# Kernel optimization log

Hardware: AMD Instinct MI355X
Metric: run time of the kernel (lower is better)

Reference implementation:

```python
import jax, jax.numpy as jnp
import numpy as np
from jax import lax

L, H, DH, D, FF = 8, 16, 64, 1024, 4096  # layers, heads, head dim, model dim, mlp hidden
B, S = 4, 512
EPS = 1e-5


def setup_inputs() -> dict:
    key = jax.random.key(0)
    ks = jax.random.split(key, 8)
    std = 0.02
    return {
        "x": jax.random.normal(ks[0], (B, S, D), jnp.float32),
        "ln1_w": jnp.ones((L, D), jnp.float32),
        "ln1_b": jnp.zeros((L, D), jnp.float32),
        "qw": jax.random.normal(ks[1], (L, H, DH, DH), jnp.float32) * std,
        "qb": jnp.zeros((L, H, DH), jnp.float32),
        "kw": jax.random.normal(ks[2], (L, H, DH, DH), jnp.float32) * std,
        "kb": jnp.zeros((L, H, DH), jnp.float32),
        "vw": jax.random.normal(ks[3], (L, H, DH, DH), jnp.float32) * std,
        "vb": jnp.zeros((L, H, DH), jnp.float32),
        "ln2_w": jnp.ones((L, D), jnp.float32),
        "ln2_b": jnp.zeros((L, D), jnp.float32),
        "w1": jax.random.normal(ks[4], (L, D, FF), jnp.float32) * std,
        "b1": jnp.zeros((L, FF), jnp.float32),
        "w2": jax.random.normal(ks[5], (L, FF, D), jnp.float32) * std,
        "b2": jnp.zeros((L, D), jnp.float32),
    }


def _layernorm(x, w, b):
    m = jnp.mean(x, axis=-1, keepdims=True)
    v = jnp.mean(jnp.square(x - m), axis=-1, keepdims=True)
    return (x - m) * lax.rsqrt(v + EPS) * w + b


def reference(x, ln1_w, ln1_b, qw, qb, kw, kb, vw, vb, ln2_w, ln2_b, w1, b1, w2, b2):
    b, s, d = x.shape
    scale = 1.0 / jnp.sqrt(jnp.asarray(DH, x.dtype))

    def layer(h, p):
        (l1w, l1b, Qw, Qb, Kw, Kb, Vw, Vb, l2w, l2b, W1, B1, W2, B2) = p
        y = _layernorm(h, l1w, l1b)
        yh = y.reshape(b, s, H, DH)
        # nn.Linear per head: y @ W.T + b, W is [out=e, in=d]
        q = jnp.einsum('bshd,hed->bshe', yh, Qw) + Qb
        k = jnp.einsum('bshd,hed->bshe', yh, Kw) + Kb
        v = jnp.einsum('bshd,hed->bshe', yh, Vw) + Vb
        attn = jax.nn.softmax(jnp.einsum('bshe,bthe->bhst', q, k) * scale, axis=-1)
        o = jnp.einsum('bhst,bthe->bshe', attn, v).reshape(b, s, d)
        h = h + o
        z = _layernorm(h, l2w, l2b)
        z = jax.nn.gelu(z @ W1 + B1, approximate=False) @ W2 + B2
        return h + z, None

    params = (ln1_w, ln1_b, qw, qb, kw, kb, vw, vb, ln2_w, ln2_b, w1, b1, w2, b2)
    out, _ = lax.scan(layer, x, params)
    return out
```

## Files before the change

kernel.cpp:

```cpp
#include <hip/hip_runtime.h>
#include <hip/hip_bf16.h>

typedef __hip_bfloat16 bf16;
typedef __bf16 bf16x8 __attribute__((ext_vector_type(8)));
typedef float f32x4 __attribute__((ext_vector_type(4)));
typedef unsigned short u16;
typedef unsigned int u32;

#define SEQ 512
#define DMODEL 1024
#define FFDIM 4096
#define NHEAD 16
#define HDIM 64
#define NB 4
#define NLAYER 8

#define SBAR() asm volatile("s_barrier" ::: "memory")

__device__ __forceinline__ u16 f2bu(float f) {
    union { bf16 h; u16 u; } c; c.h = __float2bfloat16(f); return c.u;
}

__device__ __forceinline__ void gload16(const bf16* g, bf16* l) {
    __builtin_amdgcn_global_load_lds(
        (const __attribute__((address_space(1))) unsigned int*)g,
        (__attribute__((address_space(3))) unsigned int*)l,
        16, 0, 0);
}

__device__ __forceinline__ void gemm_pipe(
    const bf16* __restrict__ A, int lda,
    const bf16* __restrict__ B, int ldb,
    int nkt,
    f32x4 (&acc)[8][2],
    char* lA, char* lB)
{
    const int tid = threadIdx.x;
    const int lane = tid & 63;
    const int wave = tid >> 6;
    const int wr = wave >> 2, wc = wave & 3;
    const int l15 = lane & 15, l4 = lane >> 4;

    auto stage = [&](int c, int t) {
        const bf16* Ak = A + t * 64;
        const bf16* Bk = B + t * 64;
        bf16* dA = (bf16*)(lA + c * 32768);
        bf16* dB = (bf16*)(lB + c * 16384);
#pragma unroll
        for (int it = 0; it < 4; ++it) {
            const int e = (it * 512 + tid) * 8;
            const int r = e >> 6;
            const int cb = (e & 63) * 2;
            const int sc = (cb ^ (((r >> 2) & 1) << 5)) >> 1;
            gload16(Ak + (long)r * lda + sc, dA + e);
        }
#pragma unroll
        for (int it = 0; it < 2; ++it) {
            const int e = (it * 512 + tid) * 8;
            const int r = e >> 6;
            const int cb = (e & 63) * 2;
            const int sc = (cb ^ (((r >> 2) & 1) << 5)) >> 1;
            gload16(Bk + (long)r * ldb + sc, dB + e);
        }
    };

    stage(0, 0);
    stage(1, 1);
    asm volatile("s_waitcnt vmcnt(6)" ::: "memory");
    SBAR();

    for (int t = 0; t < nkt; ++t) {
        const int cur = t & 1;
        const char* bA = lA + cur * 32768;
        const char* bB = lB + cur * 16384;

        bf16x8 bf_[2][2];
#pragma unroll
        for (int fn = 0; fn < 2; ++fn)
#pragma unroll
            for (int ks = 0; ks < 2; ++ks) {
                const int row = wc * 32 + fn * 16 + l15;
                int byte = row * 128 + (ks * 32 + l4 * 8) * 2;
                byte ^= ((row >> 2) & 1) << 5;
                bf_[fn][ks] = *(const bf16x8*)(bB + byte);
            }
#pragma unroll
        for (int q = 0; q < 4; ++q) {
            bf16x8 af[2][2];
#pragma unroll
            for (int i = 0; i < 2; ++i)
#pragma unroll
                for (int ks = 0; ks < 2; ++ks) {
                    const int row = wr * 128 + (q * 2 + i) * 16 + l15;
                    int byte = row * 128 + (ks * 32 + l4 * 8) * 2;
                    byte ^= ((row >> 2) & 1) << 5;
                    af[i][ks] = *(const bf16x8*)(bA + byte);
                }
            __builtin_amdgcn_s_setprio(1);
#pragma unroll
            for (int i = 0; i < 2; ++i)
#pragma unroll
                for (int fn = 0; fn < 2; ++fn)
#pragma unroll
                    for (int ks = 0; ks < 2; ++ks)
                        acc[q * 2 + i][fn] = __builtin_amdgcn_mfma_f32_16x16x32_bf16(
                            af[i][ks], bf_[fn][ks], acc[q * 2 + i][fn], 0, 0, 0);
            __builtin_amdgcn_s_setprio(0);
        }
        SBAR();
        if (t + 2 < nkt) {
            stage(cur, t + 2);
            asm volatile("s_waitcnt vmcnt(6)" ::: "memory");
        } else {
            asm volatile("s_waitcnt vmcnt(0)" ::: "memory");
        }
        SBAR();
    }
}

__global__ __launch_bounds__(256) void k_ln(const float* __restrict__ h,
                                            const float* __restrict__ w,
                                            const float* __restrict__ bp,
                                            bf16* __restrict__ out)
{
    const int row = blockIdx.x;
    const int tid = threadIdx.x;
    const float4 x = ((const float4*)(h + (long)row * DMODEL))[tid];
    float s  = x.x + x.y + x.z + x.w;
    float s2 = x.x * x.x + x.y * x.y + x.z * x.z + x.w * x.w;
#pragma unroll
    for (int off = 32; off; off >>= 1) { s += __shfl_xor(s, off); s2 += __shfl_xor(s2, off); }
    __shared__ float rs[4], rs2[4];
    const int wave = tid >> 6;
    if ((tid & 63) == 0) { rs[wave] = s; rs2[wave] = s2; }
    __syncthreads();
    const float S1 = rs[0] + rs[1] + rs[2] + rs[3];
    const float S2 = rs2[0] + rs2[1] + rs2[2] + rs2[3];
    const float mean = S1 * (1.0f / DMODEL);
    const float var  = S2 * (1.0f / DMODEL) - mean * mean;
    const float rstd = rsqrtf(var + 1e-5f);
    const float4 wv = ((const float4*)w)[tid];
    const float4 bv = ((const float4*)bp)[tid];
    uint2 o;
    o.x = (u32)f2bu((x.x - mean) * rstd * wv.x + bv.x) |
          ((u32)f2bu((x.y - mean) * rstd * wv.y + bv.y) << 16);
    o.y = (u32)f2bu((x.z - mean) * rstd * wv.z + bv.z) |
          ((u32)f2bu((x.w - mean) * rstd * wv.w + bv.w) << 16);
    ((uint2*)(out + (long)row * DMODEL))[tid] = o;
}

__global__ __launch_bounds__(256) void k_transw_all(const float* __restrict__ w1,
                                                    const float* __restrict__ w2,
                                                    bf16* __restrict__ w1t,
                                                    bf16* __restrict__ w2t)
{
    int bid = blockIdx.x;
    const int l = bid >> 11;
    bid &= 2047;
    const long lofs = (long)l * DMODEL * FFDIM;
    const float* src; bf16* dst; int R, C, rb, cb;
    if (bid < 1024) {
        src = w1 + lofs; dst = w1t + lofs; R = DMODEL; C = FFDIM;
        rb = (bid >> 6) << 6; cb = (bid & 63) << 6;
    } else {
        bid -= 1024;
        src = w2 + lofs; dst = w2t + lofs; R = FFDIM; C = DMODEL;
        rb = (bid >> 4) << 6; cb = (bid & 15) << 6;
    }
    const int tid = threadIdx.x;
    const int lane = tid & 63, wave = tid >> 6;
    const int r0 = ((wave & 1) << 5) + ((lane >> 3) << 2);
    const int c0 = ((wave >> 1) << 5) + ((lane & 7) << 2);

    float4 v[4];
#pragma unroll
    for (int i = 0; i < 4; ++i)
        v[i] = *(const float4*)(src + (long)(rb + r0 + i) * C + cb + c0);
#pragma unroll
    for (int j = 0; j < 4; ++j) {
        const float a0 = (&v[0].x)[j], a1 = (&v[1].x)[j];
        const float a2 = (&v[2].x)[j], a3 = (&v[3].x)[j];
        uint2 o;
        o.x = (u32)f2bu(a0) | ((u32)f2bu(a1) << 16);
        o.y = (u32)f2bu(a2) | ((u32)f2bu(a3) << 16);
        *(uint2*)(dst + (long)(cb + c0 + j) * R + rb + r0) = o;
    }
}

__global__ __launch_bounds__(256) void k_qkv2(const bf16* __restrict__ y,
                                              const float* __restrict__ qwl,
                                              const float* __restrict__ kwl,
                                              const float* __restrict__ vwl,
                                              const float* __restrict__ qb,
                                              const float* __restrict__ kb,
                                              const float* __restrict__ vb,
                                              bf16* __restrict__ qh,
                                              bf16* __restrict__ kh,
                                              bf16* __restrict__ vt)
{
    __shared__ __align__(16) char lmem[128 * 64 * 2 + 64 * 64 * 2];
    bf16* lA = (bf16*)lmem;
    char* lBb = lmem + 128 * 64 * 2;

    const int tid = threadIdx.x;
    const int lane = tid & 63, wave = tid >> 6;
    const int l15 = lane & 15, l4 = lane >> 4;
    const int z = blockIdx.y;
    const int b = z >> 4, hd = z & 15;
    const bf16* A = y + (long)b * SEQ * DMODEL + hd * HDIM + (long)blockIdx.x * 128 * DMODEL;

#pragma unroll
    for (int it = 0; it < 4; ++it) {
        const int f = (it * 256 + tid) * 8;
        const int r = f >> 6, c = f & 63;
        gload16(A + (long)r * DMODEL + c, lA + f);
    }
    __syncthreads();

    bf16x8 qa[2][2];
#pragma unroll
    for (int fm = 0; fm < 2; ++fm)
#pragma unroll
        for (int ks = 0; ks < 2; ++ks)
            qa[fm][ks] = *(const bf16x8*)(lA + (wave * 32 + fm * 16 + l15) * 64 + ks * 32 + l4 * 8);

    for (int t = 0; t < 3; ++t) {
        __syncthreads();
        const float* Bsrc = ((t == 0) ? qwl : (t == 1) ? kwl : vwl) + (long)hd * HDIM * HDIM;
#pragma unroll
        for (int it = 0; it < 4; ++it) {
            const int f = (it * 256 + tid) * 4;
            const float4 v = *(const float4*)(Bsrc + f);
            uint2 o;
            o.x = (u32)f2bu(v.x) | ((u32)f2bu(v.y) << 16);
            o.y = (u32)f2bu(v.z) | ((u32)f2bu(v.w) << 16);
            const int row = f >> 6;
            const int byte = (f << 1) ^ ((row & 7) << 4);
            *(uint2*)(lBb + byte) = o;
        }
        __syncthreads();

        bf16x8 bfr[4][2];
#pragma unroll
        for (int fn = 0; fn < 4; ++fn)
#pragma unroll
            for (int ks = 0; ks < 2; ++ks) {
                const int row = fn * 16 + l15;
                int byte = (row << 7) + ((ks * 32 + l4 * 8) << 1);
                byte ^= (row & 7) << 4;
                bfr[fn][ks] = *(const bf16x8*)(lBb + byte);
            }
        f32x4 acc[2][4] = {};
#pragma unroll
        for (int ks = 0; ks < 2; ++ks)
#pragma unroll
            for (int fm = 0; fm < 2; ++fm)
#pragma unroll
                for (int fn = 0; fn < 4; ++fn)
                    acc[fm][fn] = __builtin_amdgcn_mfma_f32_16x16x32_bf16(
                        qa[fm][ks], bfr[fn][ks], acc[fm][fn], 0, 0, 0);

        const float* bias = (t == 0) ? qb : (t == 1) ? kb : vb;
#pragma unroll
        for (int fm = 0; fm < 2; ++fm)
#pragma unroll
            for (int fn = 0; fn < 4; ++fn)
#pragma unroll
                for (int r = 0; r < 4; ++r) {
                    const int srow = blockIdx.x * 128 + wave * 32 + fm * 16 + l4 * 4 + r;
                    const int e = fn * 16 + l15;
                    float v = acc[fm][fn][r] + bias[hd * HDIM + e];
                    if (t == 0) {
                        qh[((long)z * SEQ + srow) * HDIM + e] = __float2bfloat16(v * 0.125f);
                    } else if (t == 1) {
                        kh[((long)z * SEQ + srow) * HDIM + e] = __float2bfloat16(v);
                    } else {
                        vt[((long)z * HDIM + e) * SEQ + srow] = __float2bfloat16(v);
                    }
                }
    }
}

__global__ __launch_bounds__(256) void k_flash(const bf16* __restrict__ qh,
                                               const bf16* __restrict__ kh,
                                               const bf16* __restrict__ vt,
                                               float* __restrict__ h)
{
    __shared__ __align__(16) char lmem[24576];
    bf16* lQ = (bf16*)lmem;
    char* lKb = lmem + 8192;
    char* lVb = lmem + 16384;

    const int tid = threadIdx.x;
    const int lane = tid & 63, wave = tid >> 6;
    const int l15 = lane & 15, l4 = lane >> 4;
    const int z = blockIdx.y;
    const int b = z >> 4, hd = z & 15;
    const int q0 = blockIdx.x * 64;

    const bf16* Qsrc = qh + ((long)z * SEQ + q0) * HDIM;
#pragma unroll
    for (int it = 0; it < 2; ++it) {
        const int f = (it * 256 + tid) * 8;
        gload16(Qsrc + f, lQ + f);
    }
    __syncthreads();

    bf16x8 qa[2];
#pragma unroll
    for (int ks = 0; ks < 2; ++ks)
        qa[ks] = *(const bf16x8*)(lQ + (wave * 16 + l15) * 64 + ks * 32 + l4 * 8);

    char* lPb = lmem + wave * 2048;

    f32x4 O[4] = {};
    float mrun[4], lrun[4];
#pragma unroll
    for (int r = 0; r < 4; ++r) { mrun[r] = -1e30f; lrun[r] = 0.0f; }

    for (int kv = 0; kv < SEQ / 64; ++kv) {
        __syncthreads();
        const bf16* Ksrc = kh + ((long)z * SEQ + kv * 64) * HDIM;
#pragma unroll
        for (int it = 0; it < 2; ++it) {
            const int f = (it * 256 + tid) * 8;
            const int r = f >> 6;
            const uint4 v = *(const uint4*)(Ksrc + f);
            *(uint4*)(lKb + ((f << 1) ^ ((r & 7) << 4))) = v;
        }
        const bf16* Vsrc = vt + (long)z * HDIM * SEQ + kv * 64;
#pragma unroll
        for (int it = 0; it < 2; ++it) {
            const int f = (it * 256 + tid) * 8;
            const int r = f >> 6, c = f & 63;
            const uint4 v = *(const uint4*)(Vsrc + (long)r * SEQ + c);
            *(uint4*)(lVb + ((f << 1) ^ ((r & 7) << 4))) = v;
        }
        __syncthreads();

        f32x4 sa[4];
#pragma unroll
        for (int fn = 0; fn < 4; ++fn) sa[fn] = (f32x4){0.f, 0.f, 0.f, 0.f};
#pragma unroll
        for (int ks = 0; ks < 2; ++ks)
#pragma unroll
            for (int fn = 0; fn < 4; ++fn) {
                const int row = fn * 16 + l15;
                int byte = (row << 7) + ((ks * 32 + l4 * 8) << 1);
                byte ^= (row & 7) << 4;
                const bf16x8 kb_ = *(const bf16x8*)(lKb + byte);
                sa[fn] = __builtin_amdgcn_mfma_f32_16x16x32_bf16(qa[ks], kb_, sa[fn], 0, 0, 0);
            }

#pragma unroll
        for (int r = 0; r < 4; ++r) {
            float mx = fmaxf(fmaxf(sa[0][r], sa[1][r]), fmaxf(sa[2][r], sa[3][r]));
#pragma unroll
            for (int m_ = 1; m_ < 16; m_ <<= 1) mx = fmaxf(mx, __shfl_xor(mx, m_));
            const float nm = fmaxf(mrun[r], mx);
            const float al = __expf(mrun[r] - nm);
            mrun[r] = nm;
            float p0 = __expf(sa[0][r] - nm), p1 = __expf(sa[1][r] - nm);
            float p2 = __expf(sa[2][r] - nm), p3 = __expf(sa[3][r] - nm);
            float ps = p0 + p1 + p2 + p3;
#pragma unroll
            for (int m_ = 1; m_ < 16; m_ <<= 1) ps += __shfl_xor(ps, m_);
            lrun[r] = lrun[r] * al + ps;
#pragma unroll
            for (int fn = 0; fn < 4; ++fn) O[fn][r] *= al;
            const int row = l4 * 4 + r;
            const int rsw = (row & 7) << 4;
            const int rb = row << 7;
            *(u16*)(lPb + ((rb + ((0 * 16 + l15) << 1)) ^ rsw)) = f2bu(p0);
            *(u16*)(lPb + ((rb + ((1 * 16 + l15) << 1)) ^ rsw)) = f2bu(p1);
            *(u16*)(lPb + ((rb + ((2 * 16 + l15) << 1)) ^ rsw)) = f2bu(p2);
            *(u16*)(lPb + ((rb + ((3 * 16 + l15) << 1)) ^ rsw)) = f2bu(p3);
        }

#pragma unroll
        for (int ks = 0; ks < 2; ++ks) {
            const int rowp = l15;
            int pbyte = (rowp << 7) + ((ks * 32 + l4 * 8) << 1);
            pbyte ^= (rowp & 7) << 4;
            const bf16x8 pa = *(const bf16x8*)(lPb + pbyte);
#pragma unroll
            for (int fn = 0; fn < 4; ++fn) {
                const int row = fn * 16 + l15;
                int byte = (row << 7) + ((ks * 32 + l4 * 8) << 1);
                byte ^= (row & 7) << 4;
                const bf16x8 vb_ = *(const bf16x8*)(lVb + byte);
                O[fn] = __builtin_amdgcn_mfma_f32_16x16x32_bf16(pa, vb_, O[fn], 0, 0, 0);
            }
        }
    }

    float rinv[4];
#pragma unroll
    for (int r = 0; r < 4; ++r) rinv[r] = 1.0f / lrun[r];
#pragma unroll
    for (int fn = 0; fn < 4; ++fn)
#pragma unroll
        for (int r = 0; r < 4; ++r) {
            const int srow = q0 + wave * 16 + l4 * 4 + r;
            const int e = fn * 16 + l15;
            h[((long)b * SEQ + srow) * DMODEL + hd * HDIM + e] += O[fn][r] * rinv[r];
        }
}

__global__ __launch_bounds__(512, 2) void k_gemm1(const bf16* __restrict__ zb,
                                                  const bf16* __restrict__ w1t,
                                                  const float* __restrict__ b1,
                                                  bf16* __restrict__ ff1)
{
    __shared__ __align__(16) char lmem[98304];
    const bf16* A = zb + (long)blockIdx.x * 256 * DMODEL;
    const bf16* B = w1t + (long)blockIdx.y * 128 * DMODEL;
    f32x4 acc[8][2] = {};
    gemm_pipe(A, DMODEL, B, DMODEL, DMODEL / 64, acc, lmem, lmem + 65536);

    const int lane = threadIdx.x & 63, wave = threadIdx.x >> 6;
    const int wr = wave >> 2, wc = wave & 3;
    const int l15 = lane & 15, l4 = lane >> 4;
#pragma unroll
    for (int fm = 0; fm < 8; ++fm)
#pragma unroll
        for (int fn = 0; fn < 2; ++fn)
#pragma unroll
            for (int r = 0; r < 4; ++r) {
                const int row = blockIdx.x * 256 + wr * 128 + fm * 16 + l4 * 4 + r;
                const int col = blockIdx.y * 128 + wc * 32 + fn * 16 + l15;
                const float x = acc[fm][fn][r] + b1[col];
                const float g = 0.5f * x * (1.0f + erff(x * 0.70710678118f));
                ff1[(long)row * FFDIM + col] = __float2bfloat16(g);
            }
}

__global__ __launch_bounds__(512, 2) void k_gemm2(const bf16* __restrict__ ff1,
                                                  const bf16* __restrict__ w2t,
                                                  float* __restrict__ part)
{
    __shared__ __align__(16) char lmem[98304];
    const int sk = blockIdx.z;
    const bf16* A = ff1 + (long)blockIdx.x * 256 * FFDIM + (long)sk * 1024;
    const bf16* B = w2t + (long)blockIdx.y * 128 * FFDIM + (long)sk * 1024;
    f32x4 acc[8][2] = {};
    gemm_pipe(A, FFDIM, B, FFDIM, 1024 / 64, acc, lmem, lmem + 65536);

    float* out = part + (long)sk * (NB * SEQ) * DMODEL;
    const int lane = threadIdx.x & 63, wave = threadIdx.x >> 6;
    const int wr = wave >> 2, wc = wave & 3;
    const int l15 = lane & 15, l4 = lane >> 4;
#pragma unroll
    for (int fm = 0; fm < 8; ++fm)
#pragma unroll
        for (int fn = 0; fn < 2; ++fn)
#pragma unroll
            for (int r = 0; r < 4; ++r) {
                const int row = blockIdx.x * 256 + wr * 128 + fm * 16 + l4 * 4 + r;
                const int col = blockIdx.y * 128 + wc * 32 + fn * 16 + l15;
                out[(long)row * DMODEL + col] = acc[fm][fn][r];
            }
}

__global__ __launch_bounds__(256) void k_red2ln(const float* __restrict__ part,
                                                const float* __restrict__ b2,
                                                float* __restrict__ h,
                                                const float* __restrict__ lnw,
                                                const float* __restrict__ lnb,
                                                bf16* __restrict__ y,
                                                int do_ln)
{
    constexpr long NELT = (long)NB * SEQ * DMODEL / 4;
    const long row = blockIdx.x;
    const int tid = threadIdx.x;
    const long i = row * (DMODEL / 4) + tid;
    float4 s = ((const float4*)part)[i];
    const float4 s1 = ((const float4*)part)[i + NELT];
    const float4 s2 = ((const float4*)part)[i + 2 * NELT];
    const float4 s3 = ((const float4*)part)[i + 3 * NELT];
    const float4 bv = ((const float4*)b2)[tid];
    float4 hv = ((float4*)h)[i];
    hv.x += s.x + s1.x + s2.x + s3.x + bv.x;
    hv.y += s.y + s1.y + s2.y + s3.y + bv.y;
    hv.z += s.z + s1.z + s2.z + s3.z + bv.z;
    hv.w += s.w + s1.w + s2.w + s3.w + bv.w;
    ((float4*)h)[i] = hv;

    if (!do_ln) return;
    float ss  = hv.x + hv.y + hv.z + hv.w;
    float ss2 = hv.x * hv.x + hv.y * hv.y + hv.z * hv.z + hv.w * hv.w;
#pragma unroll
    for (int off = 32; off; off >>= 1) { ss += __shfl_xor(ss, off); ss2 += __shfl_xor(ss2, off); }
    __shared__ float rs[4], rs2[4];
    const int wave = tid >> 6;
    if ((tid & 63) == 0) { rs[wave] = ss; rs2[wave] = ss2; }
    __syncthreads();
    const float S1 = rs[0] + rs[1] + rs[2] + rs[3];
    const float S2 = rs2[0] + rs2[1] + rs2[2] + rs2[3];
    const float mean = S1 * (1.0f / DMODEL);
    const float var  = S2 * (1.0f / DMODEL) - mean * mean;
    const float rstd = rsqrtf(var + 1e-5f);
    const float4 wv = ((const float4*)lnw)[tid];
    const float4 lb = ((const float4*)lnb)[tid];
    uint2 o;
    o.x = (u32)f2bu((hv.x - mean) * rstd * wv.x + lb.x) |
          ((u32)f2bu((hv.y - mean) * rstd * wv.y + lb.y) << 16);
    o.y = (u32)f2bu((hv.z - mean) * rstd * wv.z + lb.z) |
          ((u32)f2bu((hv.w - mean) * rstd * wv.w + lb.w) << 16);
    ((uint2*)(y + row * DMODEL))[tid] = o;
}

extern "C" void kernel_launch(void* const* d_in, const int* in_sizes, int n_in,
                              void* d_out, int out_size, void* d_ws, size_t ws_size,
                              hipStream_t stream)
{
    const float* x    = (const float*)d_in[0];
    const float* ln1w = (const float*)d_in[1];
    const float* ln1b = (const float*)d_in[2];
    const float* qw   = (const float*)d_in[3];
    const float* qb   = (const float*)d_in[4];
    const float* kw   = (const float*)d_in[5];
    const float* kb   = (const float*)d_in[6];
    const float* vw   = (const float*)d_in[7];
    const float* vb   = (const float*)d_in[8];
    const float* ln2w = (const float*)d_in[9];
    const float* ln2b = (const float*)d_in[10];
    const float* w1   = (const float*)d_in[11];
    const float* b1   = (const float*)d_in[12];
    const float* w2   = (const float*)d_in[13];
    const float* b2   = (const float*)d_in[14];

    char* ws = (char*)d_ws;
    const size_t MB = 1024 * 1024;
    bf16* y    = (bf16*)(ws + 0 * MB);
    bf16* zb   = (bf16*)(ws + 4 * MB);
    bf16* qh   = (bf16*)(ws + 8 * MB);
    bf16* kh   = (bf16*)(ws + 12 * MB);
    bf16* vt   = (bf16*)(ws + 16 * MB);
    bf16* ff1  = (bf16*)(ws + 20 * MB);
    float* part = (float*)(ws + 36 * MB);
    bf16* w1tA = (bf16*)(ws + 68 * MB);
    bf16* w2tA = (bf16*)(ws + 132 * MB);

    float* h = (float*)d_out;
    hipMemcpyAsync(d_out, x, (size_t)NB * SEQ * DMODEL * sizeof(float),
                   hipMemcpyDeviceToDevice, stream);

    k_transw_all<<<NLAYER * 2048, 256, 0, stream>>>(w1, w2, w1tA, w2tA);
    k_ln<<<NB * SEQ, 256, 0, stream>>>(x, ln1w, ln1b, y);

    for (int l = 0; l < NLAYER; ++l) {
        const long wofs = (long)l * DMODEL * FFDIM;
        k_qkv2<<<dim3(4, NB * NHEAD), 256, 0, stream>>>(
            y, qw + (long)l * 65536, kw + (long)l * 65536, vw + (long)l * 65536,
            qb + l * NHEAD * HDIM, kb + l * NHEAD * HDIM, vb + l * NHEAD * HDIM,
            qh, kh, vt);
        k_flash<<<dim3(SEQ / 64, NB * NHEAD), 256, 0, stream>>>(qh, kh, vt, h);
        k_ln<<<NB * SEQ, 256, 0, stream>>>(h, ln2w + l * DMODEL, ln2b + l * DMODEL, zb);
        k_gemm1<<<dim3(8, 32), 512, 0, stream>>>(zb, w1tA + wofs, b1 + l * FFDIM, ff1);
        k_gemm2<<<dim3(8, 8, 4), 512, 0, stream>>>(ff1, w2tA + wofs, part);
        const int last = (l == NLAYER - 1);
        k_red2ln<<<NB * SEQ, 256, 0, stream>>>(part, b2 + l * DMODEL, h,
                                               ln1w + (l + 1) * DMODEL * (1 - last),
                                               ln1b + (l + 1) * DMODEL * (1 - last),
                                               y, !last);
    }
}
```

Baseline: 952.0 us.

## Restructure GEMM pipeline, bf16 split-K partials, remap grids, fold residual copy

Several unrelated changes land together. The GEMM main loop now loads all A fragments up front, waits on LDS, issues the next stage's global loads before the MFMA block, and then runs all 32 MFMAs in one prioritized burst, aiming for better load/compute overlap. The split-K partials of gemm2 are stored as bf16 instead of fp32, halving partial-sum write and read traffic in the reduction kernel at some cost in accuracy. The block-index mappings of both GEMMs are swizzled to change L2 reuse order, and the initial residual memcpy is folded into the first layernorm kernel.

```diff
diff --git a/kernel.cpp b/kernel.cpp
--- a/kernel.cpp
+++ b/kernel.cpp
@@ -20,6 +20,9 @@
 __device__ __forceinline__ u16 f2bu(float f) {
     union { bf16 h; u16 u; } c; c.h = __float2bfloat16(f); return c.u;
 }
+__device__ __forceinline__ float bu2f(u16 u) {
+    union { u32 i; float f; } c; c.i = ((u32)u) << 16; return c.f;
+}
 
 __device__ __forceinline__ void gload16(const bf16* g, bf16* l) {
     __builtin_amdgcn_global_load_lds(
@@ -74,7 +77,7 @@
         const char* bA = lA + cur * 32768;
         const char* bB = lB + cur * 16384;
 
-        bf16x8 bf_[2][2];
+        bf16x8 bf_[2][2], af[8][2];
 #pragma unroll
         for (int fn = 0; fn < 2; ++fn)
 #pragma unroll
@@ -85,31 +88,31 @@
                 bf_[fn][ks] = *(const bf16x8*)(bB + byte);
             }
 #pragma unroll
-        for (int q = 0; q < 4; ++q) {
-            bf16x8 af[2][2];
-#pragma unroll
-            for (int i = 0; i < 2; ++i)
-#pragma unroll
-                for (int ks = 0; ks < 2; ++ks) {
-                    const int row = wr * 128 + (q * 2 + i) * 16 + l15;
-                    int byte = row * 128 + (ks * 32 + l4 * 8) * 2;
-                    byte ^= ((row >> 2) & 1) << 5;
-                    af[i][ks] = *(const bf16x8*)(bA + byte);
-                }
-            __builtin_amdgcn_s_setprio(1);
-#pragma unroll
-            for (int i = 0; i < 2; ++i)
-#pragma unroll
-                for (int fn = 0; fn < 2; ++fn)
-#pragma unroll
-                    for (int ks = 0; ks < 2; ++ks)
-                        acc[q * 2 + i][fn] = __builtin_amdgcn_mfma_f32_16x16x32_bf16(
-                            af[i][ks], bf_[fn][ks], acc[q * 2 + i][fn], 0, 0, 0);
-            __builtin_amdgcn_s_setprio(0);
-        }
+        for (int i = 0; i < 8; ++i)
+#pragma unroll
+            for (int ks = 0; ks < 2; ++ks) {
+                const int row = wr * 128 + i * 16 + l15;
+                int byte = row * 128 + (ks * 32 + l4 * 8) * 2;
+                byte ^= ((row >> 2) & 1) << 5;
+                af[i][ks] = *(const bf16x8*)(bA + byte);
+            }
+        asm volatile("s_waitcnt lgkmcnt(0)" ::: "memory");
+        __builtin_amdgcn_sched_barrier(0);
         SBAR();
+        if (t + 2 < nkt) stage(cur, t + 2);
+
+        __builtin_amdgcn_s_setprio(1);
+#pragma unroll
+        for (int i = 0; i < 8; ++i)
+#pragma unroll
+            for (int fn = 0; fn < 2; ++fn)
+#pragma unroll
+                for (int ks = 0; ks < 2; ++ks)
+                    acc[i][fn] = __builtin_amdgcn_mfma_f32_16x16x32_bf16(
+                        af[i][ks], bf_[fn][ks], acc[i][fn], 0, 0, 0);
+        __builtin_amdgcn_s_setprio(0);
+
         if (t + 2 < nkt) {
-            stage(cur, t + 2);
             asm volatile("s_waitcnt vmcnt(6)" ::: "memory");
         } else {
             asm volatile("s_waitcnt vmcnt(0)" ::: "memory");
@@ -121,11 +124,13 @@
 __global__ __launch_bounds__(256) void k_ln(const float* __restrict__ h,
                                             const float* __restrict__ w,
                                             const float* __restrict__ bp,
-                                            bf16* __restrict__ out)
+                                            bf16* __restrict__ out,
+                                            float* __restrict__ hcopy)
 {
     const int row = blockIdx.x;
     const int tid = threadIdx.x;
     const float4 x = ((const float4*)(h + (long)row * DMODEL))[tid];
+    if (hcopy) ((float4*)(hcopy + (long)row * DMODEL))[tid] = x;
     float s  = x.x + x.y + x.z + x.w;
     float s2 = x.x * x.x + x.y * x.y + x.z * x.z + x.w * x.w;
 #pragma unroll
@@ -413,8 +418,10 @@
                                                   bf16* __restrict__ ff1)
 {
     __shared__ __align__(16) char lmem[98304];
-    const bf16* A = zb + (long)blockIdx.x * 256 * DMODEL;
-    const bf16* B = w1t + (long)blockIdx.y * 128 * DMODEL;
+    const int bx = (int)blockIdx.y >> 2;
+    const int by = (int)blockIdx.x * 4 + ((int)blockIdx.y & 3);
+    const bf16* A = zb + (long)bx * 256 * DMODEL;
+    const bf16* B = w1t + (long)by * 128 * DMODEL;
     f32x4 acc[8][2] = {};
     gemm_pipe(A, DMODEL, B, DMODEL, DMODEL / 64, acc, lmem, lmem + 65536);
 
@@ -427,8 +434,8 @@
         for (int fn = 0; fn < 2; ++fn)
 #pragma unroll
             for (int r = 0; r < 4; ++r) {
-                const int row = blockIdx.x * 256 + wr * 128 + fm * 16 + l4 * 4 + r;
-                const int col = blockIdx.y * 128 + wc * 32 + fn * 16 + l15;
+                const int row = bx * 256 + wr * 128 + fm * 16 + l4 * 4 + r;
+                const int col = by * 128 + wc * 32 + fn * 16 + l15;
                 const float x = acc[fm][fn][r] + b1[col];
                 const float g = 0.5f * x * (1.0f + erff(x * 0.70710678118f));
                 ff1[(long)row * FFDIM + col] = __float2bfloat16(g);
@@ -437,16 +444,18 @@
 
 __global__ __launch_bounds__(512, 2) void k_gemm2(const bf16* __restrict__ ff1,
                                                   const bf16* __restrict__ w2t,
-                                                  float* __restrict__ part)
+                                                  bf16* __restrict__ part)
 {
     __shared__ __align__(16) char lmem[98304];
     const int sk = blockIdx.z;
-    const bf16* A = ff1 + (long)blockIdx.x * 256 * FFDIM + (long)sk * 1024;
-    const bf16* B = w2t + (long)blockIdx.y * 128 * FFDIM + (long)sk * 1024;
+    const int bx = (int)blockIdx.y;
+    const int by = (int)blockIdx.x;
+    const bf16* A = ff1 + (long)bx * 256 * FFDIM + (long)sk * 1024;
+    const bf16* B = w2t + (long)by * 128 * FFDIM + (long)sk * 1024;
     f32x4 acc[8][2] = {};
     gemm_pipe(A, FFDIM, B, FFDIM, 1024 / 64, acc, lmem, lmem + 65536);
 
-    float* out = part + (long)sk * (NB * SEQ) * DMODEL;
+    bf16* out = part + (long)sk * (NB * SEQ) * DMODEL;
     const int lane = threadIdx.x & 63, wave = threadIdx.x >> 6;
     const int wr = wave >> 2, wc = wave & 3;
     const int l15 = lane & 15, l4 = lane >> 4;
@@ -456,13 +465,13 @@
         for (int fn = 0; fn < 2; ++fn)
 #pragma unroll
             for (int r = 0; r < 4; ++r) {
-                const int row = blockIdx.x * 256 + wr * 128 + fm * 16 + l4 * 4 + r;
-                const int col = blockIdx.y * 128 + wc * 32 + fn * 16 + l15;
-                out[(long)row * DMODEL + col] = acc[fm][fn][r];
-            }
-}
-
-__global__ __launch_bounds__(256) void k_red2ln(const float* __restrict__ part,
+                const int row = bx * 256 + wr * 128 + fm * 16 + l4 * 4 + r;
+                const int col = by * 128 + wc * 32 + fn * 16 + l15;
+                out[(long)row * DMODEL + col] = __float2bfloat16(acc[fm][fn][r]);
+            }
+}
+
+__global__ __launch_bounds__(256) void k_red2ln(const bf16* __restrict__ part,
                                                 const float* __restrict__ b2,
                                                 float* __restrict__ h,
                                                 const float* __restrict__ lnw,
@@ -470,21 +479,26 @@
                                                 bf16* __restrict__ y,
                                                 int do_ln)
 {
-    constexpr long NELT = (long)NB * SEQ * DMODEL / 4;
+    constexpr long NELT = (long)NB * SEQ * DMODEL;
     const long row = blockIdx.x;
     const int tid = threadIdx.x;
-    const long i = row * (DMODEL / 4) + tid;
-    float4 s = ((const float4*)part)[i];
-    const float4 s1 = ((const float4*)part)[i + NELT];
-    const float4 s2 = ((const float4*)part)[i + 2 * NELT];
-    const float4 s3 = ((const float4*)part)[i + 3 * NELT];
+    const long e0 = row * DMODEL + tid * 4;
+    float sum[4] = {0.f, 0.f, 0.f, 0.f};
+#pragma unroll
+    for (int sk = 0; sk < 4; ++sk) {
+        const uint2 u = *(const uint2*)(part + sk * NELT + e0);
+        sum[0] += bu2f((u16)(u.x & 0xffffu));
+        sum[1] += bu2f((u16)(u.x >> 16));
+        sum[2] += bu2f((u16)(u.y & 0xffffu));
+        sum[3] += bu2f((u16)(u.y >> 16));
+    }
     const float4 bv = ((const float4*)b2)[tid];
-    float4 hv = ((float4*)h)[i];
-    hv.x += s.x + s1.x + s2.x + s3.x + bv.x;
-    hv.y += s.y + s1.y + s2.y + s3.y + bv.y;
-    hv.z += s.z + s1.z + s2.z + s3.z + bv.z;
-    hv.w += s.w + s1.w + s2.w + s3.w + bv.w;
-    ((float4*)h)[i] = hv;
+    float4 hv = ((float4*)h)[row * (DMODEL / 4) + tid];
+    hv.x += sum[0] + bv.x;
+    hv.y += sum[1] + bv.y;
+    hv.z += sum[2] + bv.z;
+    hv.w += sum[3] + bv.w;
+    ((float4*)h)[row * (DMODEL / 4) + tid] = hv;
 
     if (!do_ln) return;
     float ss  = hv.x + hv.y + hv.z + hv.w;
@@ -538,16 +552,14 @@
     bf16* kh   = (bf16*)(ws + 12 * MB);
     bf16* vt   = (bf16*)(ws + 16 * MB);
     bf16* ff1  = (bf16*)(ws + 20 * MB);
-    float* part = (float*)(ws + 36 * MB);
+    bf16* part = (bf16*)(ws + 36 * MB);
     bf16* w1tA = (bf16*)(ws + 68 * MB);
     bf16* w2tA = (bf16*)(ws + 132 * MB);
 
     float* h = (float*)d_out;
-    hipMemcpyAsync(d_out, x, (size_t)NB * SEQ * DMODEL * sizeof(float),
-                   hipMemcpyDeviceToDevice, stream);
 
     k_transw_all<<<NLAYER * 2048, 256, 0, stream>>>(w1, w2, w1tA, w2tA);
-    k_ln<<<NB * SEQ, 256, 0, stream>>>(x, ln1w, ln1b, y);
+    k_ln<<<NB * SEQ, 256, 0, stream>>>(x, ln1w, ln1b, y, h);
 
     for (int l = 0; l < NLAYER; ++l) {
         const long wofs = (long)l * DMODEL * FFDIM;
@@ -556,7 +568,8 @@
             qb + l * NHEAD * HDIM, kb + l * NHEAD * HDIM, vb + l * NHEAD * HDIM,
             qh, kh, vt);
         k_flash<<<dim3(SEQ / 64, NB * NHEAD), 256, 0, stream>>>(qh, kh, vt, h);
-        k_ln<<<NB * SEQ, 256, 0, stream>>>(h, ln2w + l * DMODEL, ln2b + l * DMODEL, zb);
+        k_ln<<<NB * SEQ, 256, 0, stream>>>(h, ln2w + l * DMODEL, ln2b + l * DMODEL, zb,
+                                           nullptr);
         k_gemm1<<<dim3(8, 32), 512, 0, stream>>>(zb, w1tA + wofs, b1 + l * FFDIM, ff1);
         k_gemm2<<<dim3(8, 8, 4), 512, 0, stream>>>(ff1, w2tA + wofs, part);
         const int last = (l == NLAYER - 1);
```

Result: slower. 992.3 us (+4.2%).
